# Kernel optimization log

Measured on AMD Instinct MI355X. Metric: run time of the kernel, lower is better.

## Reference

```python
import jax, jax.numpy as jnp
import numpy as np

B, T, D = 2, 2048, 1024
G, E, F = 4, 4, 4096          # num_groups, experts_per_group, d_ff
KG, KE = 2, 1                  # top_k_groups, top_k_experts


def setup_inputs() -> dict:
    key = jax.random.key(0)
    ks = jax.random.split(key, 5)
    init = lambda k, shape, fan: jax.random.normal(k, shape, jnp.float32) / np.sqrt(fan).astype(np.float32)
    x = jax.random.normal(ks[0], (B, T, D), jnp.float32)
    Wg = init(ks[1], (G, D), D)          # group router (torch Linear weight [out,in])
    We = init(ks[2], (G, E, D), D)       # per-group expert routers
    W1 = init(ks[3], (G, E, F, D), D)    # expert up-proj weights
    W2 = init(ks[4], (G, E, D, F), F)    # expert down-proj weights
    return {"x": x, "Wg": Wg, "We": We, "W1": W1, "W2": W2}


def _moe_forward(x, Wg, We, W1, W2):
    b, t, d = x.shape
    xf = x.reshape(b * t, d)                                   # [N, D]
    group_logits = xf @ Wg.T                                   # [N, G]
    gw, gid = jax.lax.top_k(group_logits, KG)                  # [N, KG]
    gw = jax.nn.softmax(gw, axis=-1)
    expert_logits = jnp.einsum('nd,ged->nge', xf, We)          # [N, G, E]
    sel = jnp.take_along_axis(expert_logits, gid[:, :, None], axis=1)  # [N, KG, E]
    ew, eid = jax.lax.top_k(sel, KE)                           # [N, KG, KE]
    ew = jax.nn.softmax(ew, axis=-1)
    w = gw[:, :, None] * ew                                    # [N, KG, KE]
    oh_g = jax.nn.one_hot(gid, G, dtype=xf.dtype)              # [N, KG, G]
    oh_e = jax.nn.one_hot(eid, E, dtype=xf.dtype)              # [N, KG, KE, E]
    # topk group ids are distinct, and expert ids within a group are distinct,
    # so this scatter-by-one-hot exactly reproduces the masked accumulation.
    combine = jnp.einsum('nrg,nrke,nrk->nge', oh_g, oh_e, w)   # [N, G, E]
    out = jnp.zeros_like(xf)
    for g in range(G):
        for e in range(E):
            h = jax.nn.gelu(xf @ W1[g, e].T, approximate=False)  # exact GELU, as nn.GELU()
            out = out + combine[:, g, e, None] * (h @ W2[g, e].T)
    return out.reshape(b, t, d), group_logits.reshape(b, t, G)


def reference(x, Wg, We, W1, W2):
    out, group_logits = _moe_forward(x, Wg, We, W1, W2)
    p = jax.nn.softmax(group_logits, axis=-1)
    lp = jax.nn.log_softmax(group_logits, axis=-1)
    group_entropy = -(p * lp).sum(-1).mean()
    return out, group_logits, group_entropy
```

## Files before the change

### kernel.cpp

```cpp
#include <hip/hip_runtime.h>
#include <hip/hip_bf16.h>

#define NTOK 4096
#define DDIM 1024
#define GG 4
#define EE 4
#define FF 4096
#define NEXP 16
#define OUT_ELEMS 4194304
#define GL_OFF 4194304
#define ENT_OFF 4210688

typedef float f32x4 __attribute__((ext_vector_type(4)));
typedef short short8 __attribute__((ext_vector_type(8)));

__device__ inline unsigned short f2bf(float f) {
  unsigned int u = __float_as_uint(f);
  unsigned int rounding = 0x7FFFu + ((u >> 16) & 1u);
  return (unsigned short)((u + rounding) >> 16);
}
__device__ inline unsigned int pack2(float f0, float f1) {
  return (unsigned int)f2bf(f0) | ((unsigned int)f2bf(f1) << 16);
}

__global__ void cvt_kernel(const float* __restrict__ x, unsigned short* __restrict__ xb) {
  int idx = blockIdx.x * 256 + threadIdx.x;
  const float4* p = reinterpret_cast<const float4*>(x) + (size_t)idx * 2;
  float4 a = p[0], b = p[1];
  uint4 v;
  v.x = pack2(a.x, a.y); v.y = pack2(a.z, a.w);
  v.z = pack2(b.x, b.y); v.w = pack2(b.z, b.w);
  reinterpret_cast<uint4*>(xb)[idx] = v;
}

__global__ __launch_bounds__(256) void routing_kernel(
    const float* __restrict__ x, const float* __restrict__ Wg,
    const float* __restrict__ We, float* __restrict__ out,
    int* __restrict__ cnt, int* __restrict__ tokL, int* __restrict__ hrwL,
    float* __restrict__ wslot) {
  int wave = threadIdx.x >> 6, lane = threadIdx.x & 63;
  int token = blockIdx.x * 4 + wave;
  const float4* xr = reinterpret_cast<const float4*>(x + (size_t)token * DDIM);
  float4 xv[4];
#pragma unroll
  for (int c = 0; c < 4; c++) xv[c] = xr[c * 64 + lane];

  auto dotrow = [&](const float* w) -> float {
    const float4* w4 = reinterpret_cast<const float4*>(w);
    float s = 0.f;
#pragma unroll
    for (int c = 0; c < 4; c++) {
      float4 wv = w4[c * 64 + lane];
      s += xv[c].x * wv.x + xv[c].y * wv.y + xv[c].z * wv.z + xv[c].w * wv.w;
    }
#pragma unroll
    for (int off = 32; off; off >>= 1) s += __shfl_xor(s, off, 64);
    return s;
  };

  float gl[GG];
#pragma unroll
  for (int g = 0; g < GG; g++) gl[g] = dotrow(Wg + g * DDIM);

  int g0 = 0;
  for (int g = 1; g < GG; g++) if (gl[g] > gl[g0]) g0 = g;
  int g1 = -1;
  for (int g = 0; g < GG; g++) { if (g == g0) continue; if (g1 < 0 || gl[g] > gl[g1]) g1 = g; }
  float e1 = __expf(gl[g1] - gl[g0]);
  float inv = 1.f / (1.f + e1);
  float w0 = inv, w1 = e1 * inv;

  int gsel[2] = {g0, g1};
  float wsel[2] = {w0, w1};
  int esel[2];
#pragma unroll
  for (int r = 0; r < 2; r++) {
    float el[EE];
#pragma unroll
    for (int e = 0; e < EE; e++) el[e] = dotrow(We + ((size_t)gsel[r] * EE + e) * DDIM);
    int best = 0;
    for (int e = 1; e < EE; e++) if (el[e] > el[best]) best = e;
    esel[r] = best;
  }

  float m = gl[0];
  for (int g = 1; g < GG; g++) m = fmaxf(m, gl[g]);
  float se = 0.f;
  for (int g = 0; g < GG; g++) se += __expf(gl[g] - m);
  float lse = __logf(se);
  float ent = 0.f;
  for (int g = 0; g < GG; g++) {
    float lp = gl[g] - m - lse;
    ent -= __expf(lp) * lp;
  }

  if (lane == 0) {
    for (int g = 0; g < GG; g++) out[GL_OFF + token * GG + g] = gl[g];
    atomicAdd(out + ENT_OFF, ent * (1.0f / NTOK));
    for (int r = 0; r < 2; r++) {
      int ge = gsel[r] * EE + esel[r];
      int pos = atomicAdd(cnt + ge, 1);
      tokL[ge * NTOK + pos] = token;
      hrwL[ge * NTOK + pos] = r * NTOK + token;
      wslot[r * NTOK + token] = wsel[r];
    }
  }
}

#define LDSP 40

__global__ __launch_bounds__(256) void up_kernel(
    const unsigned short* __restrict__ xb, const float* __restrict__ W1,
    const int* __restrict__ cnt, const int* __restrict__ tokL,
    const int* __restrict__ hrwL, unsigned short* __restrict__ H) {
  int ge = blockIdx.z, mt = blockIdx.y;
  int count = cnt[ge];
  if (mt * 64 >= count) return;
  int f0 = blockIdx.x * 64;

  __shared__ short As[64 * LDSP];
  __shared__ short Bs[64 * LDSP];
  __shared__ int rowsS[64];
  __shared__ int destS[64];

  int t = threadIdx.x;
  if (t < 64) {
    int i = mt * 64 + t;
    bool valid = i < count;
    rowsS[t] = valid ? tokL[ge * NTOK + i] : 0;
    destS[t] = valid ? hrwL[ge * NTOK + i] : -1;
  }
  __syncthreads();

  int srow = t >> 2;
  int schunk = (t & 3) * 8;
  const unsigned short* aptr = xb + (size_t)rowsS[srow] * DDIM + schunk;
  const float* bptr = W1 + ((size_t)ge * FF + (f0 + srow)) * DDIM + schunk;
  short* aw = &As[srow * LDSP + schunk];
  short* bw = &Bs[srow * LDSP + schunk];

  int wv = t >> 6, lane = t & 63;
  int m0 = wv * 16;
  int kg = (lane >> 4) * 8;
  const short8* afp = reinterpret_cast<const short8*>(&As[(m0 + (lane & 15)) * LDSP + kg]);

  f32x4 acc[4] = {};

  for (int kb = 0; kb < DDIM; kb += 32) {
    uint4 av = *reinterpret_cast<const uint4*>(aptr + kb);
    float4 b0 = *reinterpret_cast<const float4*>(bptr + kb);
    float4 b1 = *reinterpret_cast<const float4*>(bptr + kb + 4);
    *reinterpret_cast<uint4*>(aw) = av;
    uint4 bv;
    bv.x = pack2(b0.x, b0.y); bv.y = pack2(b0.z, b0.w);
    bv.z = pack2(b1.x, b1.y); bv.w = pack2(b1.z, b1.w);
    *reinterpret_cast<uint4*>(bw) = bv;
    __syncthreads();
    short8 af = *afp;
#pragma unroll
    for (int j = 0; j < 4; j++) {
      short8 bf = *reinterpret_cast<const short8*>(&Bs[(j * 16 + (lane & 15)) * LDSP + kg]);
      acc[j] = __builtin_amdgcn_mfma_f32_16x16x32_bf16(af, bf, acc[j], 0, 0, 0);
    }
    __syncthreads();
  }

  int rl = (lane >> 4) * 4;
  int col = lane & 15;
#pragma unroll
  for (int j = 0; j < 4; j++) {
    int f = f0 + j * 16 + col;
#pragma unroll
    for (int i2 = 0; i2 < 4; i2++) {
      int hr = destS[m0 + rl + i2];
      if (hr >= 0) {
        float v = acc[j][i2];
        float gel = 0.5f * v * (1.0f + erff(v * 0.70710678118654752f));
        H[(size_t)hr * FF + f] = f2bf(gel);
      }
    }
  }
}

__global__ __launch_bounds__(256) void down_kernel(
    const unsigned short* __restrict__ H, const float* __restrict__ W2,
    const int* __restrict__ cnt, const int* __restrict__ hrwL,
    float* __restrict__ Y) {
  int ge = blockIdx.z, mt = blockIdx.y;
  int count = cnt[ge];
  if (mt * 64 >= count) return;
  int d0 = blockIdx.x * 64;

  __shared__ short As[64 * LDSP];
  __shared__ short Bs[64 * LDSP];
  __shared__ int rowsS[64];

  int t = threadIdx.x;
  if (t < 64) {
    int i = mt * 64 + t;
    bool valid = i < count;
    rowsS[t] = valid ? hrwL[ge * NTOK + i] : -1;
  }
  __syncthreads();

  int srow = t >> 2;
  int schunk = (t & 3) * 8;
  int arow = rowsS[srow] < 0 ? 0 : rowsS[srow];
  const unsigned short* aptr = H + (size_t)arow * FF + schunk;
  const float* bptr = W2 + ((size_t)ge * DDIM + (d0 + srow)) * FF + schunk;
  short* aw = &As[srow * LDSP + schunk];
  short* bw = &Bs[srow * LDSP + schunk];

  int wv = t >> 6, lane = t & 63;
  int m0 = wv * 16;
  int kg = (lane >> 4) * 8;
  const short8* afp = reinterpret_cast<const short8*>(&As[(m0 + (lane & 15)) * LDSP + kg]);

  f32x4 acc[4] = {};

  for (int kb = 0; kb < FF; kb += 32) {
    uint4 av = *reinterpret_cast<const uint4*>(aptr + kb);
    float4 b0 = *reinterpret_cast<const float4*>(bptr + kb);
    float4 b1 = *reinterpret_cast<const float4*>(bptr + kb + 4);
    *reinterpret_cast<uint4*>(aw) = av;
    uint4 bv;
    bv.x = pack2(b0.x, b0.y); bv.y = pack2(b0.z, b0.w);
    bv.z = pack2(b1.x, b1.y); bv.w = pack2(b1.z, b1.w);
    *reinterpret_cast<uint4*>(bw) = bv;
    __syncthreads();
    short8 af = *afp;
#pragma unroll
    for (int j = 0; j < 4; j++) {
      short8 bf = *reinterpret_cast<const short8*>(&Bs[(j * 16 + (lane & 15)) * LDSP + kg]);
      acc[j] = __builtin_amdgcn_mfma_f32_16x16x32_bf16(af, bf, acc[j], 0, 0, 0);
    }
    __syncthreads();
  }

  int rl = (lane >> 4) * 4;
  int col = lane & 15;
#pragma unroll
  for (int j = 0; j < 4; j++) {
    int d = d0 + j * 16 + col;
#pragma unroll
    for (int i2 = 0; i2 < 4; i2++) {
      int hr = rowsS[m0 + rl + i2];
      if (hr >= 0) Y[(size_t)hr * DDIM + d] = acc[j][i2];
    }
  }
}

__global__ void combine_kernel(const float* __restrict__ Y,
                               const float* __restrict__ wslot,
                               float* __restrict__ out) {
  int idx = blockIdx.x * 256 + threadIdx.x;
  int token = idx >> 8;
  float w0 = wslot[token], w1 = wslot[NTOK + token];
  float4 a = reinterpret_cast<const float4*>(Y)[idx];
  float4 b = reinterpret_cast<const float4*>(Y + (size_t)NTOK * DDIM)[idx];
  float4 o;
  o.x = w0 * a.x + w1 * b.x;
  o.y = w0 * a.y + w1 * b.y;
  o.z = w0 * a.z + w1 * b.z;
  o.w = w0 * a.w + w1 * b.w;
  reinterpret_cast<float4*>(out)[idx] = o;
}

extern "C" void kernel_launch(void* const* d_in, const int* in_sizes, int n_in,
                              void* d_out, int out_size, void* d_ws, size_t ws_size,
                              hipStream_t stream) {
  const float* x  = (const float*)d_in[0];
  const float* Wg = (const float*)d_in[1];
  const float* We = (const float*)d_in[2];
  const float* W1 = (const float*)d_in[3];
  const float* W2 = (const float*)d_in[4];
  float* out = (float*)d_out;
  char* ws = (char*)d_ws;

  int* cnt = (int*)(ws);
  int* tokL = (int*)(ws + 1024);
  int* hrwL = (int*)(ws + 1024 + 262144);
  float* wslot = (float*)(ws + 1024 + 524288);
  unsigned short* xb = (unsigned short*)(ws + (1 << 20));
  unsigned short* H  = (unsigned short*)(ws + (1 << 20) + 8388608);
  float* Y = (float*)(ws + (1 << 20) + 8388608 + 67108864);

  hipMemsetAsync(d_out, 0, (size_t)out_size * sizeof(float), stream);
  hipMemsetAsync(ws, 0, 1024, stream);

  cvt_kernel<<<2048, 256, 0, stream>>>(x, xb);
  routing_kernel<<<1024, 256, 0, stream>>>(x, Wg, We, out, cnt, tokL, hrwL, wslot);
  up_kernel<<<dim3(FF / 64, 64, NEXP), 256, 0, stream>>>(xb, W1, cnt, tokL, hrwL, H);
  down_kernel<<<dim3(DDIM / 64, 64, NEXP), 256, 0, stream>>>(H, W2, cnt, hrwL, Y);
  combine_kernel<<<4096, 256, 0, stream>>>(Y, wslot, out);
}
```

Measured before the change: 1.100 ms.

## Unify expert GEMMs into 128x128-tiled template with direct-to-LDS loads and prefetch

```diff
diff --git a/kernel.cpp b/kernel.cpp
--- a/kernel.cpp
+++ b/kernel.cpp
@@ -7,7 +7,6 @@
 #define EE 4
 #define FF 4096
 #define NEXP 16
-#define OUT_ELEMS 4194304
 #define GL_OFF 4194304
 #define ENT_OFF 4210688
 
@@ -21,6 +20,12 @@
 }
 __device__ inline unsigned int pack2(float f0, float f1) {
   return (unsigned int)f2bf(f0) | ((unsigned int)f2bf(f1) << 16);
+}
+
+__device__ inline void gll16(const void* g, void* l) {
+  __builtin_amdgcn_global_load_lds(
+      (const __attribute__((address_space(1))) unsigned int*)g,
+      (__attribute__((address_space(3))) unsigned int*)l, 16, 0, 0);
 }
 
 __global__ void cvt_kernel(const float* __restrict__ x, unsigned short* __restrict__ xb) {
@@ -107,145 +112,108 @@
   }
 }
 
-#define LDSP 40
-
-__global__ __launch_bounds__(256) void up_kernel(
-    const unsigned short* __restrict__ xb, const float* __restrict__ W1,
-    const int* __restrict__ cnt, const int* __restrict__ tokL,
-    const int* __restrict__ hrwL, unsigned short* __restrict__ H) {
-  int ge = blockIdx.z, mt = blockIdx.y;
+template<int NDIM, int KDIM, bool GELU>
+__global__ __launch_bounds__(256) void moe_gemm(
+    const unsigned short* __restrict__ A,
+    const float* __restrict__ W,
+    const int* __restrict__ cnt,
+    const int* __restrict__ rows,
+    const int* __restrict__ dest,
+    unsigned short* __restrict__ outB,
+    float* __restrict__ outF) {
+  int ge = blockIdx.z;
   int count = cnt[ge];
-  if (mt * 64 >= count) return;
-  int f0 = blockIdx.x * 64;
-
-  __shared__ short As[64 * LDSP];
-  __shared__ short Bs[64 * LDSP];
-  __shared__ int rowsS[64];
-  __shared__ int destS[64];
+  int mt = blockIdx.x;
+  if (mt * 128 >= count) return;
+  int n0 = blockIdx.y * 128;
+
+  __shared__ alignas(16) short As[8 * 512];
+  __shared__ alignas(16) short Bs[8 * 512];
+  __shared__ int rowsS[128];
+  __shared__ int destS[128];
 
   int t = threadIdx.x;
-  if (t < 64) {
-    int i = mt * 64 + t;
-    bool valid = i < count;
-    rowsS[t] = valid ? tokL[ge * NTOK + i] : 0;
-    destS[t] = valid ? hrwL[ge * NTOK + i] : -1;
+  if (t < 128) {
+    int i = mt * 128 + t;
+    bool v = i < count;
+    rowsS[t] = v ? rows[ge * NTOK + i] : 0;
+    destS[t] = v ? dest[ge * NTOK + i] : -1;
   }
   __syncthreads();
 
-  int srow = t >> 2;
-  int schunk = (t & 3) * 8;
-  const unsigned short* aptr = xb + (size_t)rowsS[srow] * DDIM + schunk;
-  const float* bptr = W1 + ((size_t)ge * FF + (f0 + srow)) * DDIM + schunk;
-  short* aw = &As[srow * LDSP + schunk];
-  short* bw = &Bs[srow * LDSP + schunk];
-
-  int wv = t >> 6, lane = t & 63;
-  int m0 = wv * 16;
-  int kg = (lane >> 4) * 8;
-  const short8* afp = reinterpret_cast<const short8*>(&As[(m0 + (lane & 15)) * LDSP + kg]);
-
-  f32x4 acc[4] = {};
-
-  for (int kb = 0; kb < DDIM; kb += 32) {
-    uint4 av = *reinterpret_cast<const uint4*>(aptr + kb);
-    float4 b0 = *reinterpret_cast<const float4*>(bptr + kb);
-    float4 b1 = *reinterpret_cast<const float4*>(bptr + kb + 4);
-    *reinterpret_cast<uint4*>(aw) = av;
-    uint4 bv;
-    bv.x = pack2(b0.x, b0.y); bv.y = pack2(b0.z, b0.w);
-    bv.z = pack2(b1.x, b1.y); bv.w = pack2(b1.z, b1.w);
-    *reinterpret_cast<uint4*>(bw) = bv;
+  int lane = t & 63, w = t >> 6;
+  int i15 = lane & 15, ikg = lane >> 4;
+  int s0 = 2 * w, s1 = s0 + 1;
+
+  const unsigned short* ap0 = A + (size_t)rowsS[s0 * 16 + i15] * KDIM + ikg * 8;
+  const unsigned short* ap1 = A + (size_t)rowsS[s1 * 16 + i15] * KDIM + ikg * 8;
+  const float* bp0 = W + ((size_t)ge * NDIM + n0 + s0 * 16 + i15) * KDIM + ikg * 8;
+  const float* bp1 = W + ((size_t)ge * NDIM + n0 + s1 * 16 + i15) * KDIM + ikg * 8;
+  short* aw0 = &As[s0 * 512];
+  short* aw1 = &As[s1 * 512];
+  uint4* bw0 = reinterpret_cast<uint4*>(&Bs[s0 * 512 + lane * 8]);
+  uint4* bw1 = reinterpret_cast<uint4*>(&Bs[s1 * 512 + lane * 8]);
+
+  int wrow = w >> 1, wcol = w & 1;
+
+  f32x4 acc[4][4] = {};
+
+  float4 u0 = *reinterpret_cast<const float4*>(bp0);
+  float4 u1 = *reinterpret_cast<const float4*>(bp0 + 4);
+  float4 v0 = *reinterpret_cast<const float4*>(bp1);
+  float4 v1 = *reinterpret_cast<const float4*>(bp1 + 4);
+
+  for (int kb = 0; kb < KDIM; kb += 32) {
+    gll16(ap0 + kb, aw0);
+    gll16(ap1 + kb, aw1);
+    uint4 b0, b1;
+    b0.x = pack2(u0.x, u0.y); b0.y = pack2(u0.z, u0.w);
+    b0.z = pack2(u1.x, u1.y); b0.w = pack2(u1.z, u1.w);
+    b1.x = pack2(v0.x, v0.y); b1.y = pack2(v0.z, v0.w);
+    b1.z = pack2(v1.x, v1.y); b1.w = pack2(v1.z, v1.w);
+    *bw0 = b0;
+    *bw1 = b1;
     __syncthreads();
-    short8 af = *afp;
-#pragma unroll
-    for (int j = 0; j < 4; j++) {
-      short8 bf = *reinterpret_cast<const short8*>(&Bs[(j * 16 + (lane & 15)) * LDSP + kg]);
-      acc[j] = __builtin_amdgcn_mfma_f32_16x16x32_bf16(af, bf, acc[j], 0, 0, 0);
-    }
+    if (kb + 32 < KDIM) {
+      u0 = *reinterpret_cast<const float4*>(bp0 + kb + 32);
+      u1 = *reinterpret_cast<const float4*>(bp0 + kb + 36);
+      v0 = *reinterpret_cast<const float4*>(bp1 + kb + 32);
+      v1 = *reinterpret_cast<const float4*>(bp1 + kb + 36);
+    }
+    short8 af[4], bf[4];
+#pragma unroll
+    for (int i = 0; i < 4; i++)
+      af[i] = *reinterpret_cast<const short8*>(&As[(wrow * 4 + i) * 512 + lane * 8]);
+#pragma unroll
+    for (int j = 0; j < 4; j++)
+      bf[j] = *reinterpret_cast<const short8*>(&Bs[(wcol * 4 + j) * 512 + lane * 8]);
+#pragma unroll
+    for (int i = 0; i < 4; i++)
+#pragma unroll
+      for (int j = 0; j < 4; j++)
+        acc[i][j] = __builtin_amdgcn_mfma_f32_16x16x32_bf16(af[i], bf[j], acc[i][j], 0, 0, 0);
     __syncthreads();
   }
 
-  int rl = (lane >> 4) * 4;
-  int col = lane & 15;
-#pragma unroll
-  for (int j = 0; j < 4; j++) {
-    int f = f0 + j * 16 + col;
-#pragma unroll
-    for (int i2 = 0; i2 < 4; i2++) {
-      int hr = destS[m0 + rl + i2];
-      if (hr >= 0) {
-        float v = acc[j][i2];
-        float gel = 0.5f * v * (1.0f + erff(v * 0.70710678118654752f));
-        H[(size_t)hr * FF + f] = f2bf(gel);
+  int rl = ikg * 4;
+#pragma unroll
+  for (int i = 0; i < 4; i++) {
+#pragma unroll
+    for (int r = 0; r < 4; r++) {
+      int ml = wrow * 64 + i * 16 + rl + r;
+      int slot = destS[ml];
+      if (slot < 0) continue;
+      size_t base = (size_t)slot * NDIM + n0 + wcol * 64 + i15;
+#pragma unroll
+      for (int j = 0; j < 4; j++) {
+        float vv = acc[i][j][r];
+        if (GELU) {
+          float gel = 0.5f * vv * (1.0f + erff(vv * 0.70710678118654752f));
+          outB[base + j * 16] = f2bf(gel);
+        } else {
+          outF[base + j * 16] = vv;
+        }
       }
-    }
-  }
-}
-
-__global__ __launch_bounds__(256) void down_kernel(
-    const unsigned short* __restrict__ H, const float* __restrict__ W2,
-    const int* __restrict__ cnt, const int* __restrict__ hrwL,
-    float* __restrict__ Y) {
-  int ge = blockIdx.z, mt = blockIdx.y;
-  int count = cnt[ge];
-  if (mt * 64 >= count) return;
-  int d0 = blockIdx.x * 64;
-
-  __shared__ short As[64 * LDSP];
-  __shared__ short Bs[64 * LDSP];
-  __shared__ int rowsS[64];
-
-  int t = threadIdx.x;
-  if (t < 64) {
-    int i = mt * 64 + t;
-    bool valid = i < count;
-    rowsS[t] = valid ? hrwL[ge * NTOK + i] : -1;
-  }
-  __syncthreads();
-
-  int srow = t >> 2;
-  int schunk = (t & 3) * 8;
-  int arow = rowsS[srow] < 0 ? 0 : rowsS[srow];
-  const unsigned short* aptr = H + (size_t)arow * FF + schunk;
-  const float* bptr = W2 + ((size_t)ge * DDIM + (d0 + srow)) * FF + schunk;
-  short* aw = &As[srow * LDSP + schunk];
-  short* bw = &Bs[srow * LDSP + schunk];
-
-  int wv = t >> 6, lane = t & 63;
-  int m0 = wv * 16;
-  int kg = (lane >> 4) * 8;
-  const short8* afp = reinterpret_cast<const short8*>(&As[(m0 + (lane & 15)) * LDSP + kg]);
-
-  f32x4 acc[4] = {};
-
-  for (int kb = 0; kb < FF; kb += 32) {
-    uint4 av = *reinterpret_cast<const uint4*>(aptr + kb);
-    float4 b0 = *reinterpret_cast<const float4*>(bptr + kb);
-    float4 b1 = *reinterpret_cast<const float4*>(bptr + kb + 4);
-    *reinterpret_cast<uint4*>(aw) = av;
-    uint4 bv;
-    bv.x = pack2(b0.x, b0.y); bv.y = pack2(b0.z, b0.w);
-    bv.z = pack2(b1.x, b1.y); bv.w = pack2(b1.z, b1.w);
-    *reinterpret_cast<uint4*>(bw) = bv;
-    __syncthreads();
-    short8 af = *afp;
-#pragma unroll
-    for (int j = 0; j < 4; j++) {
-      short8 bf = *reinterpret_cast<const short8*>(&Bs[(j * 16 + (lane & 15)) * LDSP + kg]);
-      acc[j] = __builtin_amdgcn_mfma_f32_16x16x32_bf16(af, bf, acc[j], 0, 0, 0);
-    }
-    __syncthreads();
-  }
-
-  int rl = (lane >> 4) * 4;
-  int col = lane & 15;
-#pragma unroll
-  for (int j = 0; j < 4; j++) {
-    int d = d0 + j * 16 + col;
-#pragma unroll
-    for (int i2 = 0; i2 < 4; i2++) {
-      int hr = rowsS[m0 + rl + i2];
-      if (hr >= 0) Y[(size_t)hr * DDIM + d] = acc[j][i2];
     }
   }
 }
@@ -290,7 +258,9 @@
 
   cvt_kernel<<<2048, 256, 0, stream>>>(x, xb);
   routing_kernel<<<1024, 256, 0, stream>>>(x, Wg, We, out, cnt, tokL, hrwL, wslot);
-  up_kernel<<<dim3(FF / 64, 64, NEXP), 256, 0, stream>>>(xb, W1, cnt, tokL, hrwL, H);
-  down_kernel<<<dim3(DDIM / 64, 64, NEXP), 256, 0, stream>>>(H, W2, cnt, hrwL, Y);
+  moe_gemm<FF, DDIM, true><<<dim3(32, FF / 128, NEXP), 256, 0, stream>>>(
+      xb, W1, cnt, tokL, hrwL, H, nullptr);
+  moe_gemm<DDIM, FF, false><<<dim3(32, DDIM / 128, NEXP), 256, 0, stream>>>(
+      H, W2, cnt, hrwL, hrwL, nullptr, Y);
   combine_kernel<<<4096, 256, 0, stream>>>(Y, wslot, out);
 }
```

Result: slower. 3.518 ms (+219.7%).
